# Kernel optimization log

Hardware: AMD Instinct MI355X
Metric: run time of the kernel (lower is better)

## Reference

```python
import jax, jax.numpy as jnp
import numpy as np

EMBED_DIM = 1024
NUM_HEADS = 16
HEAD_DIM = EMBED_DIM // NUM_HEADS
B, T_Q, T_K = 2, 2048, 2048


def setup_inputs() -> dict:
    key = jax.random.key(0)
    ks = jax.random.split(key, 11)
    s = 1.0 / np.sqrt(EMBED_DIM)
    return {
        "query": jax.random.normal(ks[0], (B, T_Q, EMBED_DIM), jnp.float32),
        "key": jax.random.normal(ks[1], (B, T_K, EMBED_DIM), jnp.float32),
        "value": jax.random.normal(ks[2], (B, T_K, EMBED_DIM), jnp.float32),
        "Wq": jax.random.normal(ks[3], (EMBED_DIM, EMBED_DIM), jnp.float32) * s,
        "bq": jnp.zeros((EMBED_DIM,), jnp.float32),
        "Wk": jax.random.normal(ks[4], (EMBED_DIM, EMBED_DIM), jnp.float32) * s,
        "bk": jnp.zeros((EMBED_DIM,), jnp.float32),
        "Wv": jax.random.normal(ks[5], (EMBED_DIM, EMBED_DIM), jnp.float32) * s,
        "bv": jnp.zeros((EMBED_DIM,), jnp.float32),
        "Wo": jax.random.normal(ks[6], (EMBED_DIM, EMBED_DIM), jnp.float32) * s,
        "bo": jnp.zeros((EMBED_DIM,), jnp.float32),
    }


def reference(query, key, value, Wq, bq, Wk, bk, Wv, bv, Wo, bo):
    b, tq, _ = query.shape
    tk = key.shape[1]
    # projections -> [B, H, T, Dh]
    q = (query @ Wq.T + bq).reshape(b, tq, NUM_HEADS, HEAD_DIM).transpose(0, 2, 1, 3)
    k = (key @ Wk.T + bk).reshape(b, tk, NUM_HEADS, HEAD_DIM).transpose(0, 2, 1, 3)
    v = (value @ Wv.T + bv).reshape(b, tk, NUM_HEADS, HEAD_DIM).transpose(0, 2, 1, 3)
    scores = jnp.einsum("bhqd,bhkd->bhqk", q, k) / np.sqrt(HEAD_DIM)
    attn = jax.nn.softmax(scores, axis=-1)
    attn = jnp.nan_to_num(attn, nan=0.0)  # matches torch.nan_to_num; dropout is eval-mode identity
    out = jnp.einsum("bhqk,bhkd->bhqd", attn, v)
    out = out.transpose(0, 2, 1, 3).reshape(b, tq, EMBED_DIM)
    return out @ Wo.T + bo
```

## Files before the change

kernel.cpp:

```cpp
#include <hip/hip_runtime.h>
#include <hip/hip_bf16.h>
#include <cmath>


typedef short bf16x8 __attribute__((ext_vector_type(8)));
typedef short bf16x4 __attribute__((ext_vector_type(4)));
typedef float f32x4 __attribute__((ext_vector_type(4)));

#define B_ 2
#define T_ 2048
#define E_ 1024
#define H_ 16
#define DH_ 64
#define M_ 4096
#define QSCALE 0.1803368801111204f

static __device__ __forceinline__ short f2bf(float f) {
    __hip_bfloat16 h = __float2bfloat16(f);
    return *reinterpret_cast<short*>(&h);
}

static __device__ __forceinline__ short f2bf_r(float f) {
    unsigned u;
    __builtin_memcpy(&u, &f, 4);
    return (short)((u + 0x8000u) >> 16);
}

static __device__ __forceinline__ bf16x8 cvt8(const float4 a, const float4 b) {
    bf16x8 r;
    r[0] = f2bf(a.x); r[1] = f2bf(a.y); r[2] = f2bf(a.z); r[3] = f2bf(a.w);
    r[4] = f2bf(b.x); r[5] = f2bf(b.y); r[6] = f2bf(b.z); r[7] = f2bf(b.w);
    return r;
}

static __device__ __forceinline__ void async_copy16(const short* g, short* l) {
    __builtin_amdgcn_global_load_lds(
        (const __attribute__((address_space(1))) unsigned int*)g,
        (__attribute__((address_space(3))) unsigned int*)l, 16, 0, 0);
}

__global__ __launch_bounds__(256) void conv_bf16(
    const float* __restrict__ q, const float* __restrict__ k, const float* __restrict__ v,
    const float* __restrict__ wq, const float* __restrict__ wk,
    const float* __restrict__ wv, const float* __restrict__ wo,
    short* __restrict__ qo, short* __restrict__ ko, short* __restrict__ vo,
    short* __restrict__ wqo, short* __restrict__ wko,
    short* __restrict__ wvo, short* __restrict__ woo) {
    const int y = blockIdx.y;
    const float* src; short* dst; int n;
    switch (y) {
        case 0: src = q;  dst = qo;  n = M_ * E_; break;
        case 1: src = k;  dst = ko;  n = M_ * E_; break;
        case 2: src = v;  dst = vo;  n = M_ * E_; break;
        case 3: src = wq; dst = wqo; n = E_ * E_; break;
        case 4: src = wk; dst = wko; n = E_ * E_; break;
        case 5: src = wv; dst = wvo; n = E_ * E_; break;
        default: src = wo; dst = woo; n = E_ * E_; break;
    }
    const int idx = (blockIdx.x * 256 + threadIdx.x) * 8;
    if (idx >= n) return;
    const float4* p = (const float4*)(src + idx);
    *(bf16x8*)(dst + idx) = cvt8(p[0], p[1]);
}

template <int CMODE>
__device__ __forceinline__ void gemm128_tile(const short* __restrict__ A,
                                             const short* __restrict__ W,
                                             const float* __restrict__ bias,
                                             void* __restrict__ C, int bx, int by,
                                             float scale) {
    __shared__ short Asm[128 * 64];
    __shared__ short Wsm[128 * 64];
    const int tid = threadIdx.x;
    const int wave = tid >> 6, lane = tid & 63, quad = lane >> 4, l16 = lane & 15;
    const int wr = wave >> 1, wc = wave & 1;
    const int m_base = by * 128, n_base = bx * 128;
    const int xk = l16 & 7;
    const int srowA = (lane >> 3), scc = lane & 7;

    f32x4 acc[4][4] = {};

    for (int k0 = 0; k0 < E_; k0 += 64) {
#pragma unroll
        for (int i = 0; i < 4; i++) {
            const int row = i * 32 + wave * 8 + srowA;
            const int gc = (scc ^ (row & 7)) * 8;
            async_copy16(&A[(size_t)(m_base + row) * E_ + k0 + gc],
                         &Asm[(i * 256 + wave * 64) * 8]);
            async_copy16(&W[(size_t)(n_base + row) * E_ + k0 + gc],
                         &Wsm[(i * 256 + wave * 64) * 8]);
        }
        __syncthreads();

#pragma unroll
        for (int ks = 0; ks < 2; ks++) {
            bf16x8 af[4], wf[4];
#pragma unroll
            for (int i = 0; i < 4; i++) {
                const int rw = wr * 64 + i * 16 + l16;
                af[i] = *(const bf16x8*)&Asm[rw * 64 + (((ks * 4 + quad) ^ xk) * 8)];
            }
#pragma unroll
            for (int j = 0; j < 4; j++) {
                const int rw = wc * 64 + j * 16 + l16;
                wf[j] = *(const bf16x8*)&Wsm[rw * 64 + (((ks * 4 + quad) ^ xk) * 8)];
            }
#pragma unroll
            for (int i = 0; i < 4; i++)
#pragma unroll
                for (int j = 0; j < 4; j++)
                    acc[i][j] = __builtin_amdgcn_mfma_f32_16x16x32_bf16(af[i], wf[j], acc[i][j], 0, 0, 0);
        }
        __syncthreads();
    }

    if (CMODE == 2) {
#pragma unroll
        for (int j = 0; j < 4; j++) {
            const int col = n_base + wc * 64 + j * 16 + l16;
            const float bval = bias[col];
            const int h = col >> 6, d = col & 63;
#pragma unroll
            for (int i = 0; i < 4; i++) {
                const int m0 = m_base + wr * 64 + i * 16 + quad * 4;
                const int b = m0 >> 11, t0 = m0 & 2047;
                bf16x4 v;
#pragma unroll
                for (int r = 0; r < 4; r++) v[r] = f2bf(acc[i][j][r] + bval);
                *(bf16x4*)&((short*)C)[((size_t)(b * H_ + h) * DH_ + d) * T_ + t0] = v;
            }
        }
    } else {
#pragma unroll
        for (int j = 0; j < 4; j++) {
            const int col = n_base + wc * 64 + j * 16 + l16;
            const float bval = bias[col];
#pragma unroll
            for (int i = 0; i < 4; i++)
#pragma unroll
                for (int r = 0; r < 4; r++) {
                    const int m = m_base + wr * 64 + i * 16 + quad * 4 + r;
                    ((short*)C)[(size_t)m * E_ + col] = f2bf((acc[i][j][r] + bval) * scale);
                }
        }
    }
}

__global__ __launch_bounds__(256) void qkv_gemm_fast(
    const short* __restrict__ q, const short* __restrict__ k, const short* __restrict__ v,
    const short* __restrict__ Wq, const short* __restrict__ Wk, const short* __restrict__ Wv,
    const float* __restrict__ bq, const float* __restrict__ bk, const float* __restrict__ bv,
    short* __restrict__ Qb, short* __restrict__ Kb, short* __restrict__ Vtb) {
    const int z = blockIdx.z;
    if (z == 0)      gemm128_tile<0>(q, Wq, bq, Qb,  blockIdx.x, blockIdx.y, QSCALE);
    else if (z == 1) gemm128_tile<0>(k, Wk, bk, Kb,  blockIdx.x, blockIdx.y, 1.0f);
    else             gemm128_tile<2>(v, Wv, bv, Vtb, blockIdx.x, blockIdx.y, 1.0f);
}

__global__ __launch_bounds__(256) void o_gemm_fast(const short* __restrict__ A,
                                                   const short* __restrict__ W,
                                                   const float* __restrict__ bias,
                                                   float* __restrict__ C) {
    __shared__ short Asm[128 * 64];
    __shared__ short Wsm[64 * 64];
    const int tid = threadIdx.x;
    const int wave = tid >> 6, lane = tid & 63, quad = lane >> 4, l16 = lane & 15;
    const int m_base = blockIdx.y * 128, n_base = blockIdx.x * 64;
    const int xk = l16 & 7;
    const int srowA = (lane >> 3), scc = lane & 7;

    f32x4 acc[2][4] = {};

    for (int k0 = 0; k0 < E_; k0 += 64) {
#pragma unroll
        for (int i = 0; i < 4; i++) {
            const int row = i * 32 + wave * 8 + srowA;
            const int gc = (scc ^ (row & 7)) * 8;
            async_copy16(&A[(size_t)(m_base + row) * E_ + k0 + gc],
                         &Asm[(i * 256 + wave * 64) * 8]);
        }
#pragma unroll
        for (int i = 0; i < 2; i++) {
            const int row = i * 32 + wave * 8 + srowA;
            const int gc = (scc ^ (row & 7)) * 8;
            async_copy16(&W[(size_t)(n_base + row) * E_ + k0 + gc],
                         &Wsm[(i * 256 + wave * 64) * 8]);
        }
        __syncthreads();

#pragma unroll
        for (int ks = 0; ks < 2; ks++) {
            bf16x8 af[2], wf[4];
#pragma unroll
            for (int i = 0; i < 2; i++) {
                const int rw = wave * 32 + i * 16 + l16;
                af[i] = *(const bf16x8*)&Asm[rw * 64 + (((ks * 4 + quad) ^ xk) * 8)];
            }
#pragma unroll
            for (int j = 0; j < 4; j++) {
                const int rw = j * 16 + l16;
                wf[j] = *(const bf16x8*)&Wsm[rw * 64 + (((ks * 4 + quad) ^ xk) * 8)];
            }
#pragma unroll
            for (int i = 0; i < 2; i++)
#pragma unroll
                for (int j = 0; j < 4; j++)
                    acc[i][j] = __builtin_amdgcn_mfma_f32_16x16x32_bf16(af[i], wf[j], acc[i][j], 0, 0, 0);
        }
        __syncthreads();
    }

#pragma unroll
    for (int j = 0; j < 4; j++) {
        const int col = n_base + j * 16 + l16;
        const float bval = bias[col];
#pragma unroll
        for (int i = 0; i < 2; i++)
#pragma unroll
            for (int r = 0; r < 4; r++) {
                const int m = m_base + wave * 32 + i * 16 + quad * 4 + r;
                C[(size_t)m * E_ + col] = acc[i][j][r] + bval;
            }
    }
}

template <int A_BF16, int CMODE>
__device__ __forceinline__ void gemm_tile(const void* __restrict__ A,
                                          const float* __restrict__ W,
                                          const float* __restrict__ bias,
                                          void* __restrict__ C, int bx, int by,
                                          float scale) {
    __shared__ short Alds[128][40];
    __shared__ short Wlds[128][40];
    const int tid = threadIdx.x;
    const int wave = tid >> 6, lane = tid & 63, quad = lane >> 4, l16 = lane & 15;
    const int wr = wave >> 1, wc = wave & 1;
    const int m_base = by * 128, n_base = bx * 128;
    const int srow = tid >> 1, sch = (tid & 1) * 16;

    f32x4 acc[4][4] = {};

    for (int k0 = 0; k0 < E_; k0 += 32) {
        bf16x8 av0, av1, wv0, wv1;
        if (A_BF16) {
            const short* Ab = (const short*)A;
            av0 = *(const bf16x8*)&Ab[(size_t)(m_base + srow) * E_ + k0 + sch];
            av1 = *(const bf16x8*)&Ab[(size_t)(m_base + srow) * E_ + k0 + sch + 8];
        } else {
            const float4* p = (const float4*)((const float*)A +
                              (size_t)(m_base + srow) * E_ + k0 + sch);
            av0 = cvt8(p[0], p[1]);
            av1 = cvt8(p[2], p[3]);
        }
        {
            const float4* p = (const float4*)(W + (size_t)(n_base + srow) * E_ + k0 + sch);
            wv0 = cvt8(p[0], p[1]);
            wv1 = cvt8(p[2], p[3]);
        }
        *(bf16x8*)&Alds[srow][sch]     = av0;
        *(bf16x8*)&Alds[srow][sch + 8] = av1;
        *(bf16x8*)&Wlds[srow][sch]     = wv0;
        *(bf16x8*)&Wlds[srow][sch + 8] = wv1;
        __syncthreads();

        bf16x8 af[4], bfv[4];
#pragma unroll
        for (int i = 0; i < 4; i++)
            af[i] = *(const bf16x8*)&Alds[wr * 64 + i * 16 + l16][quad * 8];
#pragma unroll
        for (int j = 0; j < 4; j++)
            bfv[j] = *(const bf16x8*)&Wlds[wc * 64 + j * 16 + l16][quad * 8];
#pragma unroll
        for (int i = 0; i < 4; i++)
#pragma unroll
            for (int j = 0; j < 4; j++)
                acc[i][j] = __builtin_amdgcn_mfma_f32_16x16x32_bf16(af[i], bfv[j], acc[i][j], 0, 0, 0);
        __syncthreads();
    }

    if (CMODE == 2) {
#pragma unroll
        for (int j = 0; j < 4; j++) {
            const int col = n_base + wc * 64 + j * 16 + l16;
            const float bval = bias[col];
            const int h = col >> 6, d = col & 63;
#pragma unroll
            for (int i = 0; i < 4; i++) {
                const int m0 = m_base + wr * 64 + i * 16 + quad * 4;
                const int b = m0 >> 11, t0 = m0 & 2047;
                bf16x4 v;
#pragma unroll
                for (int r = 0; r < 4; r++) v[r] = f2bf(acc[i][j][r] + bval);
                *(bf16x4*)&((short*)C)[((size_t)(b * H_ + h) * DH_ + d) * T_ + t0] = v;
            }
        }
    } else {
#pragma unroll
        for (int j = 0; j < 4; j++) {
            const int col = n_base + wc * 64 + j * 16 + l16;
            const float bval = bias[col];
#pragma unroll
            for (int i = 0; i < 4; i++)
#pragma unroll
                for (int r = 0; r < 4; r++) {
                    const int m = m_base + wr * 64 + i * 16 + quad * 4 + r;
                    const float v = (acc[i][j][r] + bval) * scale;
                    if (CMODE == 1) ((float*)C)[(size_t)m * E_ + col] = v;
                    else            ((short*)C)[(size_t)m * E_ + col] = f2bf(v);
                }
        }
    }
}

__global__ __launch_bounds__(256) void qkv_gemm_slow(
    const float* __restrict__ q, const float* __restrict__ k, const float* __restrict__ v,
    const float* __restrict__ Wq, const float* __restrict__ Wk, const float* __restrict__ Wv,
    const float* __restrict__ bq, const float* __restrict__ bk, const float* __restrict__ bv,
    short* __restrict__ Qb, short* __restrict__ Kb, short* __restrict__ Vtb) {
    const int z = blockIdx.z;
    if (z == 0)      gemm_tile<0, 0>(q, Wq, bq, Qb,  blockIdx.x, blockIdx.y, QSCALE);
    else if (z == 1) gemm_tile<0, 0>(k, Wk, bk, Kb,  blockIdx.x, blockIdx.y, 1.0f);
    else             gemm_tile<0, 2>(v, Wv, bv, Vtb, blockIdx.x, blockIdx.y, 1.0f);
}

__global__ __launch_bounds__(256) void o_gemm_slow(const short* __restrict__ A,
                                                   const float* __restrict__ W,
                                                   const float* __restrict__ bias,
                                                   float* __restrict__ C) {
    gemm_tile<1, 1>(A, W, bias, C, blockIdx.x, blockIdx.y, 1.0f);
}

__global__ __launch_bounds__(256) void attn(short* __restrict__ QO,
                                            const short* __restrict__ Kb,
                                            const short* __restrict__ Vtb) {
    __shared__ short Kl[2][64][68];
    __shared__ short Vl[2][64][68];
    __shared__ short Pl[4][32][68];

    const int tid = threadIdx.x;
    const int wave = tid >> 6, lane = tid & 63, quad = lane >> 4, l16 = lane & 15;
    const int bh = blockIdx.x;
    const int b = bh >> 4, h = bh & 15;
    const int q0 = blockIdx.y * 128 + wave * 32;
    const size_t base = ((size_t)b * T_) * E_ + (size_t)h * DH_;
    const size_t vbase = (size_t)bh * DH_ * T_;

    bf16x8 qf[2][2];
#pragma unroll
    for (int rt = 0; rt < 2; rt++)
#pragma unroll
        for (int ks = 0; ks < 2; ks++)
            qf[rt][ks] = *(const bf16x8*)&QO[base + (size_t)(q0 + rt * 16 + l16) * E_ + ks * 32 + quad * 8];

    bf16x8 ones;
#pragma unroll
    for (int j = 0; j < 8; j++) ones[j] = (short)0x3F80;

    f32x4 oacc[2][4] = {};
    f32x4 lacc[2] = {};

    const int srow = tid >> 2;
    const int sc = (tid & 3) * 16;

    {
        const size_t krow = base + (size_t)srow * E_;
        *(bf16x8*)&Kl[0][srow][sc]     = *(const bf16x8*)&Kb[krow + sc];
        *(bf16x8*)&Kl[0][srow][sc + 8] = *(const bf16x8*)&Kb[krow + sc + 8];
        const size_t vrow = vbase + (size_t)srow * T_;
        *(bf16x8*)&Vl[0][srow][sc]     = *(const bf16x8*)&Vtb[vrow + sc];
        *(bf16x8*)&Vl[0][srow][sc + 8] = *(const bf16x8*)&Vtb[vrow + sc + 8];
    }
    __syncthreads();

    for (int it = 0; it < T_ / 64; it++) {
        const int cur = it & 1;
        const bool have = (it + 1) < T_ / 64;

        bf16x8 nk0, nk1, nv0, nv1;
        if (have) {
            const int kt = (it + 1) * 64;
            const size_t krow = base + (size_t)(kt + srow) * E_;
            nk0 = *(const bf16x8*)&Kb[krow + sc];
            nk1 = *(const bf16x8*)&Kb[krow + sc + 8];
            const size_t vrow = vbase + (size_t)srow * T_ + kt;
            nv0 = *(const bf16x8*)&Vtb[vrow + sc];
            nv1 = *(const bf16x8*)&Vtb[vrow + sc + 8];
        }

        f32x4 sacc[2][4] = {};
#pragma unroll
        for (int ks = 0; ks < 2; ks++) {
            bf16x8 kf[4];
#pragma unroll
            for (int kn = 0; kn < 4; kn++)
                kf[kn] = *(const bf16x8*)&Kl[cur][kn * 16 + l16][ks * 32 + quad * 8];
#pragma unroll
            for (int rt = 0; rt < 2; rt++)
#pragma unroll
                for (int kn = 0; kn < 4; kn++)
                    sacc[rt][kn] = __builtin_amdgcn_mfma_f32_16x16x32_bf16(qf[rt][ks], kf[kn], sacc[rt][kn], 0, 0, 0);
        }

#pragma unroll
        for (int rt = 0; rt < 2; rt++)
#pragma unroll
            for (int r = 0; r < 4; r++) {
                short* prow = &Pl[wave][rt * 16 + quad * 4 + r][0];
                prow[l16]      = f2bf_r(exp2f(sacc[rt][0][r]));
                prow[16 + l16] = f2bf_r(exp2f(sacc[rt][1][r]));
                prow[32 + l16] = f2bf_r(exp2f(sacc[rt][2][r]));
                prow[48 + l16] = f2bf_r(exp2f(sacc[rt][3][r]));
            }
        asm volatile("s_waitcnt lgkmcnt(0)" ::: "memory");

#pragma unroll
        for (int ks = 0; ks < 2; ks++) {
            bf16x8 pf[2];
#pragma unroll
            for (int rt = 0; rt < 2; rt++)
                pf[rt] = *(const bf16x8*)&Pl[wave][rt * 16 + l16][ks * 32 + quad * 8];
#pragma unroll
            for (int rt = 0; rt < 2; rt++)
                lacc[rt] = __builtin_amdgcn_mfma_f32_16x16x32_bf16(pf[rt], ones, lacc[rt], 0, 0, 0);
#pragma unroll
            for (int dn = 0; dn < 4; dn++) {
                bf16x8 vf = *(const bf16x8*)&Vl[cur][dn * 16 + l16][ks * 32 + quad * 8];
#pragma unroll
                for (int rt = 0; rt < 2; rt++)
                    oacc[rt][dn] = __builtin_amdgcn_mfma_f32_16x16x32_bf16(pf[rt], vf, oacc[rt][dn], 0, 0, 0);
            }
        }

        if (have) {
            *(bf16x8*)&Kl[cur ^ 1][srow][sc]     = nk0;
            *(bf16x8*)&Kl[cur ^ 1][srow][sc + 8] = nk1;
            *(bf16x8*)&Vl[cur ^ 1][srow][sc]     = nv0;
            *(bf16x8*)&Vl[cur ^ 1][srow][sc + 8] = nv1;
        }
        __syncthreads();
    }

    float inv[2][4];
#pragma unroll
    for (int rt = 0; rt < 2; rt++)
#pragma unroll
        for (int r = 0; r < 4; r++) inv[rt][r] = 1.0f / lacc[rt][r];

#pragma unroll
    for (int rt = 0; rt < 2; rt++)
#pragma unroll
        for (int dn = 0; dn < 4; dn++)
#pragma unroll
            for (int r = 0; r < 4; r++) {
                const float v = oacc[rt][dn][r] * inv[rt][r];
                QO[base + (size_t)(q0 + rt * 16 + quad * 4 + r) * E_ + dn * 16 + l16] = f2bf(v);
            }
}

extern "C" void kernel_launch(void* const* d_in, const int* in_sizes, int n_in,
                              void* d_out, int out_size, void* d_ws, size_t ws_size,
                              hipStream_t stream) {
    const float* query = (const float*)d_in[0];
    const float* key   = (const float*)d_in[1];
    const float* value = (const float*)d_in[2];
    const float* Wq = (const float*)d_in[3];
    const float* bq = (const float*)d_in[4];
    const float* Wk = (const float*)d_in[5];
    const float* bk = (const float*)d_in[6];
    const float* Wv = (const float*)d_in[7];
    const float* bv = (const float*)d_in[8];
    const float* Wo = (const float*)d_in[9];
    const float* bo = (const float*)d_in[10];

    const size_t NE = (size_t)M_ * E_;
    const size_t WE = (size_t)E_ * E_;

    short* Qb  = (short*)d_ws;
    short* Vtb = Qb + NE;
    short* Kb  = (short*)d_out;

    dim3 blk(256);
    const bool fast = ws_size >= (size_t)48 * 1024 * 1024;

    if (fast) {
        short* Qin = Vtb + NE;
        short* Kin = Qin + NE;
        short* Vin = Kin + NE;
        short* Wqb = Vin + NE;
        short* Wkb = Wqb + WE;
        short* Wvb = Wkb + WE;
        short* Wob = Wvb + WE;

        conv_bf16<<<dim3(2048, 7), blk, 0, stream>>>(query, key, value, Wq, Wk, Wv, Wo,
                                                     Qin, Kin, Vin, Wqb, Wkb, Wvb, Wob);
        qkv_gemm_fast<<<dim3(8, 32, 3), blk, 0, stream>>>(Qin, Kin, Vin,
                                                          Wqb, Wkb, Wvb, bq, bk, bv,
                                                          Qb, Kb, Vtb);
        attn<<<dim3(B_ * H_, T_ / 128), blk, 0, stream>>>(Qb, Kb, Vtb);
        o_gemm_fast<<<dim3(16, 32), blk, 0, stream>>>(Qb, Wob, bo, (float*)d_out);
    } else {
        qkv_gemm_slow<<<dim3(8, 32, 3), blk, 0, stream>>>(query, key, value,
                                                          Wq, Wk, Wv, bq, bk, bv,
                                                          Qb, Kb, Vtb);
        attn<<<dim3(B_ * H_, T_ / 128), blk, 0, stream>>>(Qb, Kb, Vtb);
        o_gemm_slow<<<dim3(8, 32), blk, 0, stream>>>(Qb, Wo, bo, (float*)d_out);
    }
}
```

Baseline: 247.7 us.

## Split attention over two key halves and combine partial outputs

```diff
diff --git a/kernel.cpp b/kernel.cpp
--- a/kernel.cpp
+++ b/kernel.cpp
@@ -20,10 +20,27 @@
     return *reinterpret_cast<short*>(&h);
 }
 
+static __device__ __forceinline__ float bf2f(short s) {
+    unsigned u = ((unsigned)(unsigned short)s) << 16;
+    float f;
+    __builtin_memcpy(&f, &u, 4);
+    return f;
+}
+
 static __device__ __forceinline__ short f2bf_r(float f) {
     unsigned u;
     __builtin_memcpy(&u, &f, 4);
     return (short)((u + 0x8000u) >> 16);
+}
+
+static __device__ __forceinline__ float fast_exp2(float x) {
+#if __has_builtin(__builtin_amdgcn_exp2f)
+    return __builtin_amdgcn_exp2f(x);
+#else
+    float y;
+    asm volatile("v_exp_f32 %0, %1" : "=v"(y) : "v"(x));
+    return y;
+#endif
 }
 
 static __device__ __forceinline__ bf16x8 cvt8(const float4 a, const float4 b) {
@@ -224,6 +241,284 @@
     }
 }
 
+__global__ __launch_bounds__(256) void attn_split(const short* __restrict__ Qb,
+                                                  const short* __restrict__ Kb,
+                                                  const short* __restrict__ Vtb,
+                                                  short* __restrict__ Op,
+                                                  float* __restrict__ Ls) {
+    __shared__ short Kl[2][64][68];
+    __shared__ short Vl[2][64][68];
+    __shared__ short Pl[4][32][68];
+
+    const int tid = threadIdx.x;
+    const int wave = tid >> 6, lane = tid & 63, quad = lane >> 4, l16 = lane & 15;
+    const int bh = blockIdx.x;
+    const int b = bh >> 4, h = bh & 15;
+    const int ksp = blockIdx.z;
+    const int q0 = blockIdx.y * 128 + wave * 32;
+    const int kt0 = ksp * (T_ / 2);
+    const size_t base = ((size_t)b * T_) * E_ + (size_t)h * DH_;
+    const size_t vbase = (size_t)bh * DH_ * T_;
+    short* Opk = Op + (size_t)ksp * M_ * E_;
+    float* Lsk = Ls + (size_t)ksp * 32 * T_ + (size_t)bh * T_;
+
+    bf16x8 qf[2][2];
+#pragma unroll
+    for (int rt = 0; rt < 2; rt++)
+#pragma unroll
+        for (int ks = 0; ks < 2; ks++)
+            qf[rt][ks] = *(const bf16x8*)&Qb[base + (size_t)(q0 + rt * 16 + l16) * E_ + ks * 32 + quad * 8];
+
+    bf16x8 ones;
+#pragma unroll
+    for (int j = 0; j < 8; j++) ones[j] = (short)0x3F80;
+
+    f32x4 oacc[2][4] = {};
+    f32x4 lacc[2] = {};
+
+    const int srow = tid >> 2;
+    const int sc = (tid & 3) * 16;
+
+    {
+        const size_t krow = base + (size_t)(kt0 + srow) * E_;
+        *(bf16x8*)&Kl[0][srow][sc]     = *(const bf16x8*)&Kb[krow + sc];
+        *(bf16x8*)&Kl[0][srow][sc + 8] = *(const bf16x8*)&Kb[krow + sc + 8];
+        const size_t vrow = vbase + (size_t)srow * T_ + kt0;
+        *(bf16x8*)&Vl[0][srow][sc]     = *(const bf16x8*)&Vtb[vrow + sc];
+        *(bf16x8*)&Vl[0][srow][sc + 8] = *(const bf16x8*)&Vtb[vrow + sc + 8];
+    }
+    __syncthreads();
+
+    for (int it = 0; it < T_ / 128; it++) {
+        const int cur = it & 1;
+        const bool have = (it + 1) < T_ / 128;
+
+        bf16x8 nk0, nk1, nv0, nv1;
+        if (have) {
+            const int kt = kt0 + (it + 1) * 64;
+            const size_t krow = base + (size_t)(kt + srow) * E_;
+            nk0 = *(const bf16x8*)&Kb[krow + sc];
+            nk1 = *(const bf16x8*)&Kb[krow + sc + 8];
+            const size_t vrow = vbase + (size_t)srow * T_ + kt;
+            nv0 = *(const bf16x8*)&Vtb[vrow + sc];
+            nv1 = *(const bf16x8*)&Vtb[vrow + sc + 8];
+        }
+
+        f32x4 sacc[2][4] = {};
+#pragma unroll
+        for (int ks = 0; ks < 2; ks++) {
+            bf16x8 kf[4];
+#pragma unroll
+            for (int kn = 0; kn < 4; kn++)
+                kf[kn] = *(const bf16x8*)&Kl[cur][kn * 16 + l16][ks * 32 + quad * 8];
+#pragma unroll
+            for (int rt = 0; rt < 2; rt++)
+#pragma unroll
+                for (int kn = 0; kn < 4; kn++)
+                    sacc[rt][kn] = __builtin_amdgcn_mfma_f32_16x16x32_bf16(qf[rt][ks], kf[kn], sacc[rt][kn], 0, 0, 0);
+        }
+
+#pragma unroll
+        for (int rt = 0; rt < 2; rt++)
+#pragma unroll
+            for (int r = 0; r < 4; r++) {
+                short* prow = &Pl[wave][rt * 16 + quad * 4 + r][0];
+                prow[l16]      = f2bf_r(fast_exp2(sacc[rt][0][r]));
+                prow[16 + l16] = f2bf_r(fast_exp2(sacc[rt][1][r]));
+                prow[32 + l16] = f2bf_r(fast_exp2(sacc[rt][2][r]));
+                prow[48 + l16] = f2bf_r(fast_exp2(sacc[rt][3][r]));
+            }
+        asm volatile("s_waitcnt lgkmcnt(0)" ::: "memory");
+
+#pragma unroll
+        for (int ks = 0; ks < 2; ks++) {
+            bf16x8 pf[2];
+#pragma unroll
+            for (int rt = 0; rt < 2; rt++)
+                pf[rt] = *(const bf16x8*)&Pl[wave][rt * 16 + l16][ks * 32 + quad * 8];
+#pragma unroll
+            for (int rt = 0; rt < 2; rt++)
+                lacc[rt] = __builtin_amdgcn_mfma_f32_16x16x32_bf16(pf[rt], ones, lacc[rt], 0, 0, 0);
+#pragma unroll
+            for (int dn = 0; dn < 4; dn++) {
+                bf16x8 vf = *(const bf16x8*)&Vl[cur][dn * 16 + l16][ks * 32 + quad * 8];
+#pragma unroll
+                for (int rt = 0; rt < 2; rt++)
+                    oacc[rt][dn] = __builtin_amdgcn_mfma_f32_16x16x32_bf16(pf[rt], vf, oacc[rt][dn], 0, 0, 0);
+            }
+        }
+
+        if (have) {
+            *(bf16x8*)&Kl[cur ^ 1][srow][sc]     = nk0;
+            *(bf16x8*)&Kl[cur ^ 1][srow][sc + 8] = nk1;
+            *(bf16x8*)&Vl[cur ^ 1][srow][sc]     = nv0;
+            *(bf16x8*)&Vl[cur ^ 1][srow][sc + 8] = nv1;
+        }
+        __syncthreads();
+    }
+
+#pragma unroll
+    for (int rt = 0; rt < 2; rt++) {
+#pragma unroll
+        for (int dn = 0; dn < 4; dn++)
+#pragma unroll
+            for (int r = 0; r < 4; r++)
+                Opk[base + (size_t)(q0 + rt * 16 + quad * 4 + r) * E_ + dn * 16 + l16] =
+                    f2bf(oacc[rt][dn][r]);
+        if (l16 == 0) {
+#pragma unroll
+            for (int r = 0; r < 4; r++)
+                Lsk[q0 + rt * 16 + quad * 4 + r] = lacc[rt][r];
+        }
+    }
+}
+
+__global__ __launch_bounds__(256) void combine(const short* __restrict__ Op,
+                                               const float* __restrict__ Ls,
+                                               short* __restrict__ Qb) {
+    const int idx = (blockIdx.x * 256 + threadIdx.x) * 8;
+    const int row = idx >> 10;
+    const int e = idx & 1023;
+    const int h = e >> 6;
+    const int b = row >> 11, t = row & 2047;
+    const size_t lidx = ((size_t)(b * H_ + h)) * T_ + t;
+    const float l = Ls[lidx] + Ls[(size_t)32 * T_ + lidx];
+    const float inv = 1.0f / l;
+    bf16x8 a = *(const bf16x8*)&Op[idx];
+    bf16x8 c = *(const bf16x8*)&Op[(size_t)M_ * E_ + idx];
+    bf16x8 o;
+#pragma unroll
+    for (int j = 0; j < 8; j++) o[j] = f2bf((bf2f(a[j]) + bf2f(c[j])) * inv);
+    *(bf16x8*)&Qb[idx] = o;
+}
+
+__global__ __launch_bounds__(256) void attn(short* __restrict__ QO,
+                                            const short* __restrict__ Kb,
+                                            const short* __restrict__ Vtb) {
+    __shared__ short Kl[2][64][68];
+    __shared__ short Vl[2][64][68];
+    __shared__ short Pl[4][32][68];
+
+    const int tid = threadIdx.x;
+    const int wave = tid >> 6, lane = tid & 63, quad = lane >> 4, l16 = lane & 15;
+    const int bh = blockIdx.x;
+    const int b = bh >> 4, h = bh & 15;
+    const int q0 = blockIdx.y * 128 + wave * 32;
+    const size_t base = ((size_t)b * T_) * E_ + (size_t)h * DH_;
+    const size_t vbase = (size_t)bh * DH_ * T_;
+
+    bf16x8 qf[2][2];
+#pragma unroll
+    for (int rt = 0; rt < 2; rt++)
+#pragma unroll
+        for (int ks = 0; ks < 2; ks++)
+            qf[rt][ks] = *(const bf16x8*)&QO[base + (size_t)(q0 + rt * 16 + l16) * E_ + ks * 32 + quad * 8];
+
+    bf16x8 ones;
+#pragma unroll
+    for (int j = 0; j < 8; j++) ones[j] = (short)0x3F80;
+
+    f32x4 oacc[2][4] = {};
+    f32x4 lacc[2] = {};
+
+    const int srow = tid >> 2;
+    const int sc = (tid & 3) * 16;
+
+    {
+        const size_t krow = base + (size_t)srow * E_;
+        *(bf16x8*)&Kl[0][srow][sc]     = *(const bf16x8*)&Kb[krow + sc];
+        *(bf16x8*)&Kl[0][srow][sc + 8] = *(const bf16x8*)&Kb[krow + sc + 8];
+        const size_t vrow = vbase + (size_t)srow * T_;
+        *(bf16x8*)&Vl[0][srow][sc]     = *(const bf16x8*)&Vtb[vrow + sc];
+        *(bf16x8*)&Vl[0][srow][sc + 8] = *(const bf16x8*)&Vtb[vrow + sc + 8];
+    }
+    __syncthreads();
+
+    for (int it = 0; it < T_ / 64; it++) {
+        const int cur = it & 1;
+        const bool have = (it + 1) < T_ / 64;
+
+        bf16x8 nk0, nk1, nv0, nv1;
+        if (have) {
+            const int kt = (it + 1) * 64;
+            const size_t krow = base + (size_t)(kt + srow) * E_;
+            nk0 = *(const bf16x8*)&Kb[krow + sc];
+            nk1 = *(const bf16x8*)&Kb[krow + sc + 8];
+            const size_t vrow = vbase + (size_t)srow * T_ + kt;
+            nv0 = *(const bf16x8*)&Vtb[vrow + sc];
+            nv1 = *(const bf16x8*)&Vtb[vrow + sc + 8];
+        }
+
+        f32x4 sacc[2][4] = {};
+#pragma unroll
+        for (int ks = 0; ks < 2; ks++) {
+            bf16x8 kf[4];
+#pragma unroll
+            for (int kn = 0; kn < 4; kn++)
+                kf[kn] = *(const bf16x8*)&Kl[cur][kn * 16 + l16][ks * 32 + quad * 8];
+#pragma unroll
+            for (int rt = 0; rt < 2; rt++)
+#pragma unroll
+                for (int kn = 0; kn < 4; kn++)
+                    sacc[rt][kn] = __builtin_amdgcn_mfma_f32_16x16x32_bf16(qf[rt][ks], kf[kn], sacc[rt][kn], 0, 0, 0);
+        }
+
+#pragma unroll
+        for (int rt = 0; rt < 2; rt++)
+#pragma unroll
+            for (int r = 0; r < 4; r++) {
+                short* prow = &Pl[wave][rt * 16 + quad * 4 + r][0];
+                prow[l16]      = f2bf_r(fast_exp2(sacc[rt][0][r]));
+                prow[16 + l16] = f2bf_r(fast_exp2(sacc[rt][1][r]));
+                prow[32 + l16] = f2bf_r(fast_exp2(sacc[rt][2][r]));
+                prow[48 + l16] = f2bf_r(fast_exp2(sacc[rt][3][r]));
+            }
+        asm volatile("s_waitcnt lgkmcnt(0)" ::: "memory");
+
+#pragma unroll
+        for (int ks = 0; ks < 2; ks++) {
+            bf16x8 pf[2];
+#pragma unroll
+            for (int rt = 0; rt < 2; rt++)
+                pf[rt] = *(const bf16x8*)&Pl[wave][rt * 16 + l16][ks * 32 + quad * 8];
+#pragma unroll
+            for (int rt = 0; rt < 2; rt++)
+                lacc[rt] = __builtin_amdgcn_mfma_f32_16x16x32_bf16(pf[rt], ones, lacc[rt], 0, 0, 0);
+#pragma unroll
+            for (int dn = 0; dn < 4; dn++) {
+                bf16x8 vf = *(const bf16x8*)&Vl[cur][dn * 16 + l16][ks * 32 + quad * 8];
+#pragma unroll
+                for (int rt = 0; rt < 2; rt++)
+                    oacc[rt][dn] = __builtin_amdgcn_mfma_f32_16x16x32_bf16(pf[rt], vf, oacc[rt][dn], 0, 0, 0);
+            }
+        }
+
+        if (have) {
+            *(bf16x8*)&Kl[cur ^ 1][srow][sc]     = nk0;
+            *(bf16x8*)&Kl[cur ^ 1][srow][sc + 8] = nk1;
+            *(bf16x8*)&Vl[cur ^ 1][srow][sc]     = nv0;
+            *(bf16x8*)&Vl[cur ^ 1][srow][sc + 8] = nv1;
+        }
+        __syncthreads();
+    }
+
+    float inv[2][4];
+#pragma unroll
+    for (int rt = 0; rt < 2; rt++)
+#pragma unroll
+        for (int r = 0; r < 4; r++) inv[rt][r] = 1.0f / lacc[rt][r];
+
+#pragma unroll
+    for (int rt = 0; rt < 2; rt++)
+#pragma unroll
+        for (int dn = 0; dn < 4; dn++)
+#pragma unroll
+            for (int r = 0; r < 4; r++) {
+                const float v = oacc[rt][dn][r] * inv[rt][r];
+                QO[base + (size_t)(q0 + rt * 16 + quad * 4 + r) * E_ + dn * 16 + l16] = f2bf(v);
+            }
+}
+
 template <int A_BF16, int CMODE>
 __device__ __forceinline__ void gemm_tile(const void* __restrict__ A,
                                           const float* __restrict__ W,
@@ -328,133 +623,6 @@
                                                    const float* __restrict__ bias,
                                                    float* __restrict__ C) {
     gemm_tile<1, 1>(A, W, bias, C, blockIdx.x, blockIdx.y, 1.0f);
-}
-
-__global__ __launch_bounds__(256) void attn(short* __restrict__ QO,
-                                            const short* __restrict__ Kb,
-                                            const short* __restrict__ Vtb) {
-    __shared__ short Kl[2][64][68];
-    __shared__ short Vl[2][64][68];
-    __shared__ short Pl[4][32][68];
-
-    const int tid = threadIdx.x;
-    const int wave = tid >> 6, lane = tid & 63, quad = lane >> 4, l16 = lane & 15;
-    const int bh = blockIdx.x;
-    const int b = bh >> 4, h = bh & 15;
-    const int q0 = blockIdx.y * 128 + wave * 32;
-    const size_t base = ((size_t)b * T_) * E_ + (size_t)h * DH_;
-    const size_t vbase = (size_t)bh * DH_ * T_;
-
-    bf16x8 qf[2][2];
-#pragma unroll
-    for (int rt = 0; rt < 2; rt++)
-#pragma unroll
-        for (int ks = 0; ks < 2; ks++)
-            qf[rt][ks] = *(const bf16x8*)&QO[base + (size_t)(q0 + rt * 16 + l16) * E_ + ks * 32 + quad * 8];
-
-    bf16x8 ones;
-#pragma unroll
-    for (int j = 0; j < 8; j++) ones[j] = (short)0x3F80;
-
-    f32x4 oacc[2][4] = {};
-    f32x4 lacc[2] = {};
-
-    const int srow = tid >> 2;
-    const int sc = (tid & 3) * 16;
-
-    {
-        const size_t krow = base + (size_t)srow * E_;
-        *(bf16x8*)&Kl[0][srow][sc]     = *(const bf16x8*)&Kb[krow + sc];
-        *(bf16x8*)&Kl[0][srow][sc + 8] = *(const bf16x8*)&Kb[krow + sc + 8];
-        const size_t vrow = vbase + (size_t)srow * T_;
-        *(bf16x8*)&Vl[0][srow][sc]     = *(const bf16x8*)&Vtb[vrow + sc];
-        *(bf16x8*)&Vl[0][srow][sc + 8] = *(const bf16x8*)&Vtb[vrow + sc + 8];
-    }
-    __syncthreads();
-
-    for (int it = 0; it < T_ / 64; it++) {
-        const int cur = it & 1;
-        const bool have = (it + 1) < T_ / 64;
-
-        bf16x8 nk0, nk1, nv0, nv1;
-        if (have) {
-            const int kt = (it + 1) * 64;
-            const size_t krow = base + (size_t)(kt + srow) * E_;
-            nk0 = *(const bf16x8*)&Kb[krow + sc];
-            nk1 = *(const bf16x8*)&Kb[krow + sc + 8];
-            const size_t vrow = vbase + (size_t)srow * T_ + kt;
-            nv0 = *(const bf16x8*)&Vtb[vrow + sc];
-            nv1 = *(const bf16x8*)&Vtb[vrow + sc + 8];
-        }
-
-        f32x4 sacc[2][4] = {};
-#pragma unroll
-        for (int ks = 0; ks < 2; ks++) {
-            bf16x8 kf[4];
-#pragma unroll
-            for (int kn = 0; kn < 4; kn++)
-                kf[kn] = *(const bf16x8*)&Kl[cur][kn * 16 + l16][ks * 32 + quad * 8];
-#pragma unroll
-            for (int rt = 0; rt < 2; rt++)
-#pragma unroll
-                for (int kn = 0; kn < 4; kn++)
-                    sacc[rt][kn] = __builtin_amdgcn_mfma_f32_16x16x32_bf16(qf[rt][ks], kf[kn], sacc[rt][kn], 0, 0, 0);
-        }
-
-#pragma unroll
-        for (int rt = 0; rt < 2; rt++)
-#pragma unroll
-            for (int r = 0; r < 4; r++) {
-                short* prow = &Pl[wave][rt * 16 + quad * 4 + r][0];
-                prow[l16]      = f2bf_r(exp2f(sacc[rt][0][r]));
-                prow[16 + l16] = f2bf_r(exp2f(sacc[rt][1][r]));
-                prow[32 + l16] = f2bf_r(exp2f(sacc[rt][2][r]));
-                prow[48 + l16] = f2bf_r(exp2f(sacc[rt][3][r]));
-            }
-        asm volatile("s_waitcnt lgkmcnt(0)" ::: "memory");
-
-#pragma unroll
-        for (int ks = 0; ks < 2; ks++) {
-            bf16x8 pf[2];
-#pragma unroll
-            for (int rt = 0; rt < 2; rt++)
-                pf[rt] = *(const bf16x8*)&Pl[wave][rt * 16 + l16][ks * 32 + quad * 8];
-#pragma unroll
-            for (int rt = 0; rt < 2; rt++)
-                lacc[rt] = __builtin_amdgcn_mfma_f32_16x16x32_bf16(pf[rt], ones, lacc[rt], 0, 0, 0);
-#pragma unroll
-            for (int dn = 0; dn < 4; dn++) {
-                bf16x8 vf = *(const bf16x8*)&Vl[cur][dn * 16 + l16][ks * 32 + quad * 8];
-#pragma unroll
-                for (int rt = 0; rt < 2; rt++)
-                    oacc[rt][dn] = __builtin_amdgcn_mfma_f32_16x16x32_bf16(pf[rt], vf, oacc[rt][dn], 0, 0, 0);
-            }
-        }
-
-        if (have) {
-            *(bf16x8*)&Kl[cur ^ 1][srow][sc]     = nk0;
-            *(bf16x8*)&Kl[cur ^ 1][srow][sc + 8] = nk1;
-            *(bf16x8*)&Vl[cur ^ 1][srow][sc]     = nv0;
-            *(bf16x8*)&Vl[cur ^ 1][srow][sc + 8] = nv1;
-        }
-        __syncthreads();
-    }
-
-    float inv[2][4];
-#pragma unroll
-    for (int rt = 0; rt < 2; rt++)
-#pragma unroll
-        for (int r = 0; r < 4; r++) inv[rt][r] = 1.0f / lacc[rt][r];
-
-#pragma unroll
-    for (int rt = 0; rt < 2; rt++)
-#pragma unroll
-        for (int dn = 0; dn < 4; dn++)
-#pragma unroll
-            for (int r = 0; r < 4; r++) {
-                const float v = oacc[rt][dn][r] * inv[rt][r];
-                QO[base + (size_t)(q0 + rt * 16 + quad * 4 + r) * E_ + dn * 16 + l16] = f2bf(v);
-            }
 }
 
 extern "C" void kernel_launch(void* const* d_in, const int* in_sizes, int n_in,
@@ -496,7 +664,10 @@
         qkv_gemm_fast<<<dim3(8, 32, 3), blk, 0, stream>>>(Qin, Kin, Vin,
                                                           Wqb, Wkb, Wvb, bq, bk, bv,
                                                           Qb, Kb, Vtb);
-        attn<<<dim3(B_ * H_, T_ / 128), blk, 0, stream>>>(Qb, Kb, Vtb);
+        attn_split<<<dim3(B_ * H_, T_ / 128, 2), blk, 0, stream>>>(
+            Qb, Kb, Vtb, Qin, (float*)Vin);
+        combine<<<dim3((M_ * E_) / (256 * 8)), blk, 0, stream>>>(
+            Qin, (const float*)Vin, Qb);
         o_gemm_fast<<<dim3(16, 32), blk, 0, stream>>>(Qb, Wob, bo, (float*)d_out);
     } else {
         qkv_gemm_slow<<<dim3(8, 32, 3), blk, 0, stream>>>(query, key, value,
```

After: 245.4 us. No clear change (-0.9%).
